# Performance work log

Measured on AMD Instinct MI355X. Metric: run time of the kernel, lower is better.

Reference implementation:

```python
import jax, jax.numpy as jnp
from jax import lax
import numpy as np

B, C, H, W = 4, 256, 64, 64
OC = 256
KH = KW = 3
K = KH * KW  # num_points
STRIDE, PAD, DIL = 1, 1, 1


def setup_inputs() -> dict:
    key = jax.random.key(0)
    k1, k2, k3, k4, k5 = jax.random.split(key, 5)
    x = jax.random.normal(k1, (B, C, H, W), dtype=jnp.float32)
    # offset/mask predictor conv: 3*K channels (dx, dy, mask logits). Small init so
    # offsets stay a few pixels (original inits to zero; we want nontrivial sampling).
    offset_w = jax.random.normal(k2, (3 * K, C, KH, KW), dtype=jnp.float32) * 0.01
    offset_b = jax.random.normal(k3, (3 * K,), dtype=jnp.float32) * 0.01
    fan_in = C * K
    bound = 1.0 / np.sqrt(fan_in)
    weight = jax.random.uniform(k4, (OC, C, KH, KW), dtype=jnp.float32, minval=-bound, maxval=bound)
    bias = jax.random.uniform(k5, (OC,), dtype=jnp.float32, minval=-bound, maxval=bound)
    return {"x": x, "offset_w": offset_w, "offset_b": offset_b, "weight": weight, "bias": bias}


def _bilinear_gather(x, sx, sy):
    """grid_sample(mode=bilinear, padding_mode=zeros, align_corners=True).
    x: [B,C,H,W]; sx, sy: [B,K,P] pixel-space coords. Returns [B,C,K,P].
    (align_corners=True normalize->denormalize is the identity, so we work in pixels.)
    """
    b, c, h, w = x.shape
    xf = x.reshape(b, c, h * w)
    x0 = jnp.floor(sx)
    y0 = jnp.floor(sy)
    wx1 = sx - x0
    wy1 = sy - y0
    wx0 = 1.0 - wx1
    wy0 = 1.0 - wy1

    def corner(xi, yi, wgt):
        valid = (xi >= 0) & (xi <= w - 1) & (yi >= 0) & (yi <= h - 1)
        xc = jnp.clip(xi, 0, w - 1).astype(jnp.int32)
        yc = jnp.clip(yi, 0, h - 1).astype(jnp.int32)
        idx = (yc * w + xc).reshape(b, 1, -1)  # [B,1,K*P]
        v = jnp.take_along_axis(xf, idx, axis=2).reshape(b, c, *xi.shape[1:])
        return v * (wgt * valid.astype(x.dtype))[:, None]

    out = corner(x0, y0, wx0 * wy0)
    out = out + corner(x0 + 1, y0, wx1 * wy0)
    out = out + corner(x0, y0 + 1, wx0 * wy1)
    out = out + corner(x0 + 1, y0 + 1, wx1 * wy1)
    return out


def reference(x, offset_w, offset_b, weight, bias):
    b, c, h, w = x.shape
    om = lax.conv_general_dilated(
        x, offset_w, window_strides=(STRIDE, STRIDE), padding=[(PAD, PAD), (PAD, PAD)],
        rhs_dilation=(DIL, DIL), dimension_numbers=("NCHW", "OIHW", "NCHW"))
    om = om + offset_b[None, :, None, None]
    o1, o2, m = jnp.split(om, 3, axis=1)  # each [B,K,Ho,Wo]
    ho, wo = om.shape[2], om.shape[3]
    p = ho * wo
    offx = o1.reshape(b, K, p)
    offy = o2.reshape(b, K, p)
    mask = jax.nn.sigmoid(m).reshape(b, K, p)

    # kernel grid offsets (-1..1 for k=3) and output pixel positions
    gy, gx = jnp.meshgrid(jnp.arange(-(KH // 2), KH // 2 + 1, dtype=x.dtype),
                          jnp.arange(-(KW // 2), KW // 2 + 1, dtype=x.dtype), indexing="ij")
    gx = gx.reshape(K)
    gy = gy.reshape(K)
    oy, ox = jnp.meshgrid(jnp.arange(ho, dtype=x.dtype), jnp.arange(wo, dtype=x.dtype), indexing="ij")
    ox = ox.reshape(p)
    oy = oy.reshape(p)

    sx = ox[None, None, :] * STRIDE - PAD + gx[None, :, None] * DIL + offx  # [B,K,P]
    sy = oy[None, None, :] * STRIDE - PAD + gy[None, :, None] * DIL + offy

    sampled = _bilinear_gather(x, sx, sy)            # [B,C,K,P]
    sampled = sampled * mask[:, None]                # modulation

    wmat = weight.reshape(OC, c * K)                 # [O, C*K]
    out = jnp.einsum("oi,bip->bop", wmat, sampled.reshape(b, c * K, p))
    out = out.reshape(b, OC, ho, wo) + bias[None, :, None, None]
    return out
```

## Files before the change

kernel.cpp:

```cpp
#include <hip/hip_runtime.h>


#define NB 4
#define NC 256
#define HW 64
#define NP 4096
#define NOC 256
#define NCK 2304
#define NKT 72
#define ROWB 4608

typedef __attribute__((ext_vector_type(8))) short short8;
typedef __attribute__((ext_vector_type(4))) float f32x4;
typedef unsigned short ushort_t;
typedef unsigned int uint32;

__device__ __forceinline__ void gload16(const void* g, void* l) {
    __builtin_amdgcn_global_load_lds(
        (const __attribute__((address_space(1))) unsigned int*)g,
        (__attribute__((address_space(3))) unsigned int*)l, 16, 0, 0);
}

__device__ __forceinline__ uint32 f2bf(float v) {
    uint32 b = __float_as_uint(v);
    return (b + 0x7FFFu + ((b >> 16) & 1u)) >> 16;
}
__device__ __forceinline__ float bf_lo(uint32 u) { return __uint_as_float(u << 16); }
__device__ __forceinline__ float bf_hi(uint32 u) { return __uint_as_float(u & 0xFFFF0000u); }

__global__ __launch_bounds__(256) void wprep_A(const float* __restrict__ w,
                                               ushort_t* __restrict__ wta) {
    int e = blockIdx.x * 256 + threadIdx.x;
    int o  = e / NCK;
    int ck = e - o * NCK;
    int c = ck & 255;
    int k = ck >> 8;
    wta[e] = (ushort_t)f2bf(w[o * NCK + c * 9 + k]);
}

__global__ __launch_bounds__(256) void owb_prep(const float* __restrict__ ow,
                                                ushort_t* __restrict__ owb) {
    int e = blockIdx.x * 256 + threadIdx.x;
    int c = e & 255;
    int r = e >> 8;
    int ch = r & 31;
    int k = r >> 5;
    float v = 0.f;
    if (ch < 27) v = ow[(ch * NC + c) * 9 + k];
    owb[e] = (ushort_t)f2bf(v);
}

__global__ __launch_bounds__(256) void xprep2(const float* __restrict__ x,
                                              ushort_t* __restrict__ xt) {
    __shared__ float tr[128 * 65];
    int bid = blockIdx.x;
    int pt = bid & 31;
    int cc = (bid >> 5) & 3;
    int b  = bid >> 7;
    int t = threadIdx.x;
    int c0 = cc * 64;

    const float* xb = x + ((size_t)(b * NC + c0)) * NP + pt * 128;
    #pragma unroll
    for (int pass = 0; pass < 8; ++pass) {
        int c  = pass * 8 + (t >> 5);
        int p4 = (t & 31) * 4;
        float4 v = *(const float4*)(xb + (size_t)c * NP + p4);
        tr[(p4 + 0) * 65 + c] = v.x;
        tr[(p4 + 1) * 65 + c] = v.y;
        tr[(p4 + 2) * 65 + c] = v.z;
        tr[(p4 + 3) * 65 + c] = v.w;
    }
    __syncthreads();
    ushort_t* xto = xt + ((size_t)b * NP + pt * 128) * NC + c0;
    #pragma unroll
    for (int pass = 0; pass < 4; ++pass) {
        int e = pass * 256 + t;
        int p = e >> 3, seg = e & 7;
        const float* rp = &tr[p * 65 + seg * 8];
        uint32 pk[4];
        #pragma unroll
        for (int h = 0; h < 4; ++h)
            pk[h] = f2bf(rp[2 * h]) | (f2bf(rp[2 * h + 1]) << 16);
        *(uint4*)(xto + (size_t)p * NC + seg * 8) = make_uint4(pk[0], pk[1], pk[2], pk[3]);
    }
}

__global__ __launch_bounds__(256) void offs_mfma(const ushort_t* __restrict__ xt,
                                                 const ushort_t* __restrict__ owb,
                                                 const float* __restrict__ obias,
                                                 float* __restrict__ om) {
    __shared__ __align__(16) char lds[65376];
    int bid = blockIdx.x;
    int y = bid & 63;
    int b = bid >> 6;
    int t = threadIdx.x;
    int lane = t & 63;
    int w = t >> 6;
    int r16 = lane & 15;
    int g   = lane >> 4;

    f32x4 acc[2][4];
    #pragma unroll
    for (int mf = 0; mf < 2; ++mf)
        #pragma unroll
        for (int nf = 0; nf < 4; ++nf) acc[mf][nf] = (f32x4){0.f, 0.f, 0.f, 0.f};

    const ushort_t* xtb = xt + ((size_t)b * NP) * NC;

    for (int cc = 0; cc < 4; ++cc) {
        int c0 = cc * 64;
        __syncthreads();
        for (int e = t; e < 1584; e += 256) {
            int rr = e >> 3, seg = e & 7;
            int dy = (rr >= 132) ? 2 : (rr >= 66 ? 1 : 0);
            int xx = rr - dy * 66;
            int ys = y + dy - 1;
            int xs = xx - 1;
            uint4 v = make_uint4(0, 0, 0, 0);
            if (ys >= 0 && ys < 64 && xs >= 0 && xs < 64)
                v = *(const uint4*)(xtb + ((ys << 6) + xs) * NC + c0 + seg * 8);
            *(uint4*)(lds + rr * 144 + seg * 16) = v;
        }
        for (int e = t; e < 2304; e += 256) {
            int row = e >> 3;
            int seg = e & 7;
            uint4 v = *(const uint4*)(owb + (row << 8) + c0 + seg * 8);
            *(uint4*)(lds + 28512 + (row << 7) + seg * 16) = v;
        }
        __syncthreads();
        for (int s = w; s < 9; s += 4) {
            int dy = (s >= 6) ? 2 : (s >= 3 ? 1 : 0);
            int dx = s - dy * 3;
            const char* Ab = lds + 28512 + s * 4096;
            #pragma unroll
            for (int ks = 0; ks < 2; ++ks) {
                short8 a0 = *(const short8*)(Ab + r16 * 128 + ks * 64 + g * 16);
                short8 a1 = *(const short8*)(Ab + (16 + r16) * 128 + ks * 64 + g * 16);
                #pragma unroll
                for (int nf = 0; nf < 4; ++nf) {
                    short8 bv = *(const short8*)(lds +
                        (dy * 66 + nf * 16 + r16 + dx) * 144 + ks * 64 + g * 16);
                    acc[0][nf] = __builtin_amdgcn_mfma_f32_16x16x32_bf16(
                        a0, bv, acc[0][nf], 0, 0, 0);
                    acc[1][nf] = __builtin_amdgcn_mfma_f32_16x16x32_bf16(
                        a1, bv, acc[1][nf], 0, 0, 0);
                }
            }
        }
    }
    __syncthreads();
    float* red = (float*)lds;
    #pragma unroll
    for (int mf = 0; mf < 2; ++mf)
        #pragma unroll
        for (int nf = 0; nf < 4; ++nf)
            #pragma unroll
            for (int r = 0; r < 4; ++r) {
                int ch = mf * 16 + g * 4 + r;
                int p  = nf * 16 + r16;
                red[((w * 32 + ch) << 6) + p] = acc[mf][nf][r];
            }
    __syncthreads();
    for (int e = t; e < 27 * 64; e += 256) {
        int ch = e >> 6, p = e & 63;
        float sres = red[(ch << 6) + p] + red[((32 + ch) << 6) + p]
                   + red[((64 + ch) << 6) + p] + red[((96 + ch) << 6) + p]
                   + obias[ch];
        om[((size_t)(b * 27 + ch)) * NP + (y << 6) + p] = sres;
    }
}

__global__ __launch_bounds__(256) void gather2(const ushort_t* __restrict__ xt,
                                               const float* __restrict__ om,
                                               ushort_t* __restrict__ sb) {
    __shared__ __align__(16) int   ci_l[64 * 4];
    __shared__ __align__(16) float cw_l[64 * 4];
    int g = blockIdx.x;
    int b = (g & 7) >> 1;
    int r = ((g >> 3) << 1) | (g & 1);
    int y = r & 63;
    int k = r >> 6;
    int t = threadIdx.x;

    if (t < 64) {
        int p = y * HW + t;
        const float* omb = om + ((size_t)b * 27) * NP;
        float o1 = omb[(size_t)k * NP + p];
        float o2 = omb[(size_t)(9 + k) * NP + p];
        float ml = omb[(size_t)(18 + k) * NP + p];
        float mask = 1.f / (1.f + expf(-ml));
        float sx = (float)t + (float)(k % 3) - 2.0f + o1;
        float sy = (float)y + (float)(k / 3) - 2.0f + o2;
        float x0f = floorf(sx), y0f = floorf(sy);
        float fx = sx - x0f, fy = sy - y0f;
        #pragma unroll
        for (int cy = 0; cy < 2; ++cy) {
            float yf = y0f + (float)cy;
            float wy = cy ? fy : 1.f - fy;
            #pragma unroll
            for (int cx = 0; cx < 2; ++cx) {
                float xf = x0f + (float)cx;
                float wx = cx ? fx : 1.f - fx;
                bool valid = (xf >= 0.f) && (xf <= 63.f) && (yf >= 0.f) && (yf <= 63.f);
                int xi = min(max((int)xf, 0), 63);
                int yi = min(max((int)yf, 0), 63);
                ci_l[t * 4 + cy * 2 + cx] = yi * HW + xi;
                cw_l[t * 4 + cy * 2 + cx] = valid ? wx * wy * mask : 0.f;
            }
        }
    }
    __syncthreads();

    int lane = t & 63;
    int w = t >> 6;
    const ushort_t* xtb = xt + ((size_t)b * NP) * NC + lane * 4;
    ushort_t* sbb = sb + ((size_t)b * NP + (size_t)y * HW) * NCK + k * NC + lane * 4;

    #pragma unroll 1
    for (int i = 0; i < 16; ++i) {
        int pl = w * 16 + i;
        int4   id = *(const int4*)&ci_l[pl * 4];
        float4 cw = *(const float4*)&cw_l[pl * 4];
        uint2 r0 = *(const uint2*)(xtb + (size_t)id.x * NC);
        uint2 r1 = *(const uint2*)(xtb + (size_t)id.y * NC);
        uint2 r2 = *(const uint2*)(xtb + (size_t)id.z * NC);
        uint2 r3 = *(const uint2*)(xtb + (size_t)id.w * NC);
        float s0 = cw.x*bf_lo(r0.x) + cw.y*bf_lo(r1.x) + cw.z*bf_lo(r2.x) + cw.w*bf_lo(r3.x);
        float s1 = cw.x*bf_hi(r0.x) + cw.y*bf_hi(r1.x) + cw.z*bf_hi(r2.x) + cw.w*bf_hi(r3.x);
        float s2 = cw.x*bf_lo(r0.y) + cw.y*bf_lo(r1.y) + cw.z*bf_lo(r2.y) + cw.w*bf_lo(r3.y);
        float s3 = cw.x*bf_hi(r0.y) + cw.y*bf_hi(r1.y) + cw.z*bf_hi(r2.y) + cw.w*bf_hi(r3.y);
        uint32 p0 = f2bf(s0) | (f2bf(s1) << 16);
        uint32 p1 = f2bf(s2) | (f2bf(s3) << 16);
        *(uint2*)(sbb + (size_t)pl * NCK) = make_uint2(p0, p1);
    }
}

__global__ __launch_bounds__(256) void gemm2(const ushort_t* __restrict__ wta,
                                             const ushort_t* __restrict__ sb,
                                             const float* __restrict__ bias,
                                             float* __restrict__ out) {
    __shared__ __align__(16) char lds[2 * 15360];
    int bid = blockIdx.x;
    int pt = bid & 63;
    int ot = (bid >> 6) & 1;
    int b  = bid >> 7;
    int t = threadIdx.x;
    int lane = t & 63;
    int w = t >> 6;
    int wo = w & 1;
    int wp = w >> 1;
    int r16 = lane & 15;
    int g   = lane >> 4;

    const char* Abase = (const char*)wta + (size_t)(ot * 128) * ROWB;
    const char* Bbase = (const char*)sb + (size_t)b * NP * ROWB
                                        + (size_t)(pt * 64) * ROWB;
    const char* srcp[4]; int dstp[4]; bool jv[4];
    #pragma unroll
    for (int jj = 0; jj < 4; ++jj) {
        int j = w + jj * 4;
        jv[jj] = (j < 15);
        if (j < 10) {
            int d = j * 1024 + lane * 16;
            int row = d / 80, col = d - row * 80;
            if (col >= 64) col = 48;
            srcp[jj] = Abase + (size_t)row * ROWB + col;
            dstp[jj] = j * 1024;
        } else if (j < 15) {
            int j2 = j - 10;
            int d = j2 * 1024 + lane * 16;
            int row = d / 80, col = d - row * 80;
            if (col >= 64) col = 48;
            srcp[jj] = Bbase + (size_t)row * ROWB + col;
            dstp[jj] = 10240 + j2 * 1024;
        } else { srcp[jj] = Abase; dstp[jj] = 0; }
    }

    int aoff[4], boff[2];
    #pragma unroll
    for (int f = 0; f < 4; ++f)
        aoff[f] = (wo * 64 + f * 16 + r16) * 80 + g * 16;
    #pragma unroll
    for (int f = 0; f < 2; ++f)
        boff[f] = 10240 + (wp * 32 + f * 16 + r16) * 80 + g * 16;

    f32x4 acc[4][2];
    #pragma unroll
    for (int fo = 0; fo < 4; ++fo)
        #pragma unroll
        for (int fp = 0; fp < 2; ++fp) acc[fo][fp] = (f32x4){0.f, 0.f, 0.f, 0.f};

    #pragma unroll
    for (int jj = 0; jj < 4; ++jj)
        if (jv[jj]) gload16(srcp[jj], lds + dstp[jj]);
    __syncthreads();

    for (int kt = 0; kt < NKT; ++kt) {
        int q = kt & 1;
        if (kt + 1 < NKT) {
            char* dst = lds + (q ^ 1) * 15360;
            size_t ko = (size_t)(kt + 1) * 64;
            #pragma unroll
            for (int jj = 0; jj < 4; ++jj)
                if (jv[jj]) gload16(srcp[jj] + ko, dst + dstp[jj]);
        }
        const char* buf = lds + q * 15360;
        short8 av[4], bv[2];
        #pragma unroll
        for (int f = 0; f < 4; ++f) av[f] = *(const short8*)(buf + aoff[f]);
        #pragma unroll
        for (int f = 0; f < 2; ++f) bv[f] = *(const short8*)(buf + boff[f]);
        #pragma unroll
        for (int fo = 0; fo < 4; ++fo)
            #pragma unroll
            for (int fp = 0; fp < 2; ++fp)
                acc[fo][fp] = __builtin_amdgcn_mfma_f32_16x16x32_bf16(
                    av[fo], bv[fp], acc[fo][fp], 0, 0, 0);
        __syncthreads();
    }

    int obase = ot * 128 + wo * 64;
    int pbase = pt * 64 + wp * 32 + r16;
    float* outb = out + ((size_t)b * NOC) * NP;
    #pragma unroll
    for (int fo = 0; fo < 4; ++fo) {
        #pragma unroll
        for (int rr = 0; rr < 4; ++rr) {
            int o = obase + fo * 16 + g * 4 + rr;
            float bb = bias[o];
            #pragma unroll
            for (int fp = 0; fp < 2; ++fp)
                outb[(size_t)o * NP + pbase + fp * 16] = acc[fo][fp][rr] + bb;
        }
    }
}

extern "C" void kernel_launch(void* const* d_in, const int* in_sizes, int n_in,
                              void* d_out, int out_size, void* d_ws, size_t ws_size,
                              hipStream_t stream) {
    const float* x     = (const float*)d_in[0];
    const float* ow    = (const float*)d_in[1];
    const float* obias = (const float*)d_in[2];
    const float* wgt   = (const float*)d_in[3];
    const float* bias  = (const float*)d_in[4];
    float* out = (float*)d_out;

    char* ws = (char*)d_ws;
    float*    om   = (float*)ws;
    ushort_t* owb  = (ushort_t*)(ws + 1769472);
    ushort_t* wta  = (ushort_t*)(ws + 1916928);
    ushort_t* xt   = (ushort_t*)(ws + 3096576);
    ushort_t* sbuf = (ushort_t*)(ws + 11485184);

    hipLaunchKernelGGL(wprep_A,   dim3(2304), dim3(256), 0, stream, wgt, wta);
    hipLaunchKernelGGL(owb_prep,  dim3(288),  dim3(256), 0, stream, ow, owb);
    hipLaunchKernelGGL(xprep2,    dim3(512),  dim3(256), 0, stream, x, xt);
    hipLaunchKernelGGL(offs_mfma, dim3(256),  dim3(256), 0, stream, xt, owb, obias, om);
    hipLaunchKernelGGL(gather2,   dim3(2304), dim3(256), 0, stream, xt, om, sbuf);
    hipLaunchKernelGGL(gemm2,     dim3(512),  dim3(256), 0, stream, wta, sbuf, bias, out);
}
```

Measured before the change: 173.6 us.

## Split offset conv over channel halves with atomics; widen gather loads to 16 bytes

The offset-predictor conv now splits its 256 input channels into two halves across twice as many blocks (512 instead of 256). Partial sums are combined with atomicAdd into an om buffer that a new om_init kernel pre-fills with the bias. The gather kernel now has each lane load and write 8 bf16 channels (uint4) instead of 4, halving its loop trips. This adds occupancy for the small conv grid and cuts memory instruction count in the gather, at the cost of an extra launch, atomic traffic and non-deterministic summation order.

```diff
diff --git a/kernel.cpp b/kernel.cpp
--- a/kernel.cpp
+++ b/kernel.cpp
@@ -50,6 +50,14 @@
     owb[e] = (ushort_t)f2bf(v);
 }
 
+__global__ __launch_bounds__(256) void om_init(const float* __restrict__ obias,
+                                               float* __restrict__ om) {
+    int g = blockIdx.x * 256 + threadIdx.x;
+    int r = g >> 12;
+    int ch = r % 27;
+    om[g] = obias[ch];
+}
+
 __global__ __launch_bounds__(256) void xprep2(const float* __restrict__ x,
                                               ushort_t* __restrict__ xt) {
     __shared__ float tr[128 * 65];
@@ -86,14 +94,14 @@
     }
 }
 
-__global__ __launch_bounds__(256) void offs_mfma(const ushort_t* __restrict__ xt,
-                                                 const ushort_t* __restrict__ owb,
-                                                 const float* __restrict__ obias,
-                                                 float* __restrict__ om) {
+__global__ __launch_bounds__(256) void offs_mfma2(const ushort_t* __restrict__ xt,
+                                                  const ushort_t* __restrict__ owb,
+                                                  float* __restrict__ om) {
     __shared__ __align__(16) char lds[65376];
     int bid = blockIdx.x;
-    int y = bid & 63;
-    int b = bid >> 6;
+    int h = bid & 1;
+    int y = (bid >> 1) & 63;
+    int b = bid >> 7;
     int t = threadIdx.x;
     int lane = t & 63;
     int w = t >> 6;
@@ -108,8 +116,8 @@
 
     const ushort_t* xtb = xt + ((size_t)b * NP) * NC;
 
-    for (int cc = 0; cc < 4; ++cc) {
-        int c0 = cc * 64;
+    for (int ccc = 0; ccc < 2; ++ccc) {
+        int c0 = (h * 2 + ccc) * 64;
         __syncthreads();
         for (int e = t; e < 1584; e += 256) {
             int rr = e >> 3, seg = e & 7;
@@ -165,17 +173,16 @@
     for (int e = t; e < 27 * 64; e += 256) {
         int ch = e >> 6, p = e & 63;
         float sres = red[(ch << 6) + p] + red[((32 + ch) << 6) + p]
-                   + red[((64 + ch) << 6) + p] + red[((96 + ch) << 6) + p]
-                   + obias[ch];
-        om[((size_t)(b * 27 + ch)) * NP + (y << 6) + p] = sres;
-    }
-}
-
-__global__ __launch_bounds__(256) void gather2(const ushort_t* __restrict__ xt,
+                   + red[((64 + ch) << 6) + p] + red[((96 + ch) << 6) + p];
+        atomicAdd(&om[((size_t)(b * 27 + ch)) * NP + (y << 6) + p], sres);
+    }
+}
+
+__global__ __launch_bounds__(256) void gather3(const ushort_t* __restrict__ xt,
                                                const float* __restrict__ om,
                                                ushort_t* __restrict__ sb) {
-    __shared__ __align__(16) int   ci_l[64 * 4];
-    __shared__ __align__(16) float cw_l[64 * 4];
+    __shared__ __align__(16) int4   ci_l[64];
+    __shared__ __align__(16) float4 cw_l[64];
     int g = blockIdx.x;
     int b = (g & 7) >> 1;
     int r = ((g >> 3) << 1) | (g & 1);
@@ -194,6 +201,7 @@
         float sy = (float)y + (float)(k / 3) - 2.0f + o2;
         float x0f = floorf(sx), y0f = floorf(sy);
         float fx = sx - x0f, fy = sy - y0f;
+        int idv[4]; float wgt[4];
         #pragma unroll
         for (int cy = 0; cy < 2; ++cy) {
             float yf = y0f + (float)cy;
@@ -205,34 +213,45 @@
                 bool valid = (xf >= 0.f) && (xf <= 63.f) && (yf >= 0.f) && (yf <= 63.f);
                 int xi = min(max((int)xf, 0), 63);
                 int yi = min(max((int)yf, 0), 63);
-                ci_l[t * 4 + cy * 2 + cx] = yi * HW + xi;
-                cw_l[t * 4 + cy * 2 + cx] = valid ? wx * wy * mask : 0.f;
+                idv[cy * 2 + cx] = yi * HW + xi;
+                wgt[cy * 2 + cx] = valid ? wx * wy * mask : 0.f;
             }
         }
+        ci_l[t] = make_int4(idv[0], idv[1], idv[2], idv[3]);
+        cw_l[t] = make_float4(wgt[0], wgt[1], wgt[2], wgt[3]);
     }
     __syncthreads();
 
     int lane = t & 63;
     int w = t >> 6;
-    const ushort_t* xtb = xt + ((size_t)b * NP) * NC + lane * 4;
-    ushort_t* sbb = sb + ((size_t)b * NP + (size_t)y * HW) * NCK + k * NC + lane * 4;
+    int half = lane >> 5;
+    int co = (lane & 31) * 8;
+    const ushort_t* xtb = xt + ((size_t)b * NP) * NC + co;
+    ushort_t* sbb = sb + ((size_t)b * NP + (size_t)y * HW) * NCK + k * NC + co;
 
     #pragma unroll 1
-    for (int i = 0; i < 16; ++i) {
-        int pl = w * 16 + i;
-        int4   id = *(const int4*)&ci_l[pl * 4];
-        float4 cw = *(const float4*)&cw_l[pl * 4];
-        uint2 r0 = *(const uint2*)(xtb + (size_t)id.x * NC);
-        uint2 r1 = *(const uint2*)(xtb + (size_t)id.y * NC);
-        uint2 r2 = *(const uint2*)(xtb + (size_t)id.z * NC);
-        uint2 r3 = *(const uint2*)(xtb + (size_t)id.w * NC);
-        float s0 = cw.x*bf_lo(r0.x) + cw.y*bf_lo(r1.x) + cw.z*bf_lo(r2.x) + cw.w*bf_lo(r3.x);
-        float s1 = cw.x*bf_hi(r0.x) + cw.y*bf_hi(r1.x) + cw.z*bf_hi(r2.x) + cw.w*bf_hi(r3.x);
-        float s2 = cw.x*bf_lo(r0.y) + cw.y*bf_lo(r1.y) + cw.z*bf_lo(r2.y) + cw.w*bf_lo(r3.y);
-        float s3 = cw.x*bf_hi(r0.y) + cw.y*bf_hi(r1.y) + cw.z*bf_hi(r2.y) + cw.w*bf_hi(r3.y);
-        uint32 p0 = f2bf(s0) | (f2bf(s1) << 16);
-        uint32 p1 = f2bf(s2) | (f2bf(s3) << 16);
-        *(uint2*)(sbb + (size_t)pl * NCK) = make_uint2(p0, p1);
+    for (int i = 0; i < 8; ++i) {
+        int pl = w * 16 + half * 8 + i;
+        int4   id = ci_l[pl];
+        float4 cw = cw_l[pl];
+        uint4 q0 = *(const uint4*)(xtb + (size_t)id.x * NC);
+        uint4 q1 = *(const uint4*)(xtb + (size_t)id.y * NC);
+        uint4 q2 = *(const uint4*)(xtb + (size_t)id.z * NC);
+        uint4 q3 = *(const uint4*)(xtb + (size_t)id.w * NC);
+        uint32 a0[4] = {q0.x, q0.y, q0.z, q0.w};
+        uint32 a1[4] = {q1.x, q1.y, q1.z, q1.w};
+        uint32 a2[4] = {q2.x, q2.y, q2.z, q2.w};
+        uint32 a3[4] = {q3.x, q3.y, q3.z, q3.w};
+        uint32 pk[4];
+        #pragma unroll
+        for (int d = 0; d < 4; ++d) {
+            float lo = cw.x*bf_lo(a0[d]) + cw.y*bf_lo(a1[d])
+                     + cw.z*bf_lo(a2[d]) + cw.w*bf_lo(a3[d]);
+            float hi = cw.x*bf_hi(a0[d]) + cw.y*bf_hi(a1[d])
+                     + cw.z*bf_hi(a2[d]) + cw.w*bf_hi(a3[d]);
+            pk[d] = f2bf(lo) | (f2bf(hi) << 16);
+        }
+        *(uint4*)(sbb + (size_t)pl * NCK) = make_uint4(pk[0], pk[1], pk[2], pk[3]);
     }
 }
 
@@ -353,10 +372,11 @@
     ushort_t* xt   = (ushort_t*)(ws + 3096576);
     ushort_t* sbuf = (ushort_t*)(ws + 11485184);
 
-    hipLaunchKernelGGL(wprep_A,   dim3(2304), dim3(256), 0, stream, wgt, wta);
-    hipLaunchKernelGGL(owb_prep,  dim3(288),  dim3(256), 0, stream, ow, owb);
-    hipLaunchKernelGGL(xprep2,    dim3(512),  dim3(256), 0, stream, x, xt);
-    hipLaunchKernelGGL(offs_mfma, dim3(256),  dim3(256), 0, stream, xt, owb, obias, om);
-    hipLaunchKernelGGL(gather2,   dim3(2304), dim3(256), 0, stream, xt, om, sbuf);
-    hipLaunchKernelGGL(gemm2,     dim3(512),  dim3(256), 0, stream, wta, sbuf, bias, out);
-}
+    hipLaunchKernelGGL(wprep_A,    dim3(2304), dim3(256), 0, stream, wgt, wta);
+    hipLaunchKernelGGL(owb_prep,   dim3(288),  dim3(256), 0, stream, ow, owb);
+    hipLaunchKernelGGL(om_init,    dim3(1728), dim3(256), 0, stream, obias, om);
+    hipLaunchKernelGGL(xprep2,     dim3(512),  dim3(256), 0, stream, x, xt);
+    hipLaunchKernelGGL(offs_mfma2, dim3(512),  dim3(256), 0, stream, xt, owb, om);
+    hipLaunchKernelGGL(gather3,    dim3(2304), dim3(256), 0, stream, xt, om, sbuf);
+    hipLaunchKernelGGL(gemm2,      dim3(512),  dim3(256), 0, stream, wta, sbuf, bias, out);
+}
```

Result: faster. 168.9 us (-2.7%).
